# Kernel optimization log

Measured on AMD Instinct MI355X. Metric: run time of the kernel, lower is better.

## Reference

```python
import jax, jax.numpy as jnp
import numpy as np

N = 16384          # number of nodes
FEAT = 256         # in_features
POOL_RATIO = 0.5
K = max(2, int(POOL_RATIO * N))  # 8192, static


def setup_inputs() -> dict:
    key = jax.random.key(0)
    k1, k2, k3 = jax.random.split(key, 3)
    x = jax.random.normal(k1, (N, FEAT), dtype=jnp.float32)
    # dense proxy for the adjacency matrix (source calls A.todense())
    A = jax.random.uniform(k2, (N, N), dtype=jnp.float32)
    # fc: Linear(FEAT, 1, bias=None) -> weight vector of shape [FEAT]
    W = jax.random.normal(k3, (FEAT,), dtype=jnp.float32) * (1.0 / np.sqrt(FEAT))
    return {"x": x, "A": A, "W": W}


def reference(x, A, W):
    # score = fc(dropout(x)); dropout p=0 -> identity
    score = x @ W                                   # [N]
    # global L2 normalization: score / sqrt(sum(score**2))
    score = score / jnp.sqrt(jnp.sum(score * score))
    score = jnp.tanh(score)                         # activation_gPool
    values, idx = jax.lax.top_k(score, K)           # [K], [K]
    new_x = x[idx, :] * values[:, None]             # gather + scale  [K, FEAT]
    new_A = A[idx, :][:, idx]                       # [K, K] subgraph adjacency
    return new_x, new_A, idx
```

## Files before the change

kernel.cpp:

```cpp
#include <hip/hip_runtime.h>
#include <hip/hip_bf16.h>

#define N     16384
#define FEAT  256
#define KSEL  8192
#define NCHUNK 8
#define CHUNK (N / NCHUNK)

typedef float f32x4 __attribute__((ext_vector_type(4)));

__device__ __align__(16) double g_s[N];
__device__ __align__(16) int    g_cnt[N];
__device__ __align__(16) int    g_sel[KSEL];
__device__ __align__(16) float  g_vals[KSEL];
__device__              double  g_norminv;

static __device__ __forceinline__ unsigned long long mono_key(double s) {
    unsigned long long u = (unsigned long long)__double_as_longlong(s);
    if (u & 0x8000000000000000ull) u = ~u;
    else                           u |= 0x8000000000000000ull;
    return u;
}

__global__ __launch_bounds__(512) void k_score(const float* __restrict__ x,
                                               const float* __restrict__ W) {
    int lane = threadIdx.x & 63;
    int row  = blockIdx.x * 8 + (threadIdx.x >> 6);
    float4 xv = reinterpret_cast<const float4*>(x)[row * 64 + lane];
    float4 wv = reinterpret_cast<const float4*>(W)[lane];
    double acc = (double)xv.x * (double)wv.x + (double)xv.y * (double)wv.y
               + (double)xv.z * (double)wv.z + (double)xv.w * (double)wv.w;
    #pragma unroll
    for (int m = 32; m >= 1; m >>= 1) acc += __shfl_xor(acc, m, 64);
    if (lane == 0) { g_s[row] = acc; g_cnt[row] = 0; }
}

__global__ __launch_bounds__(1024) void k_norm() {
    __shared__ double red[1024];
    double acc = 0.0;
    for (int j = threadIdx.x; j < N; j += 1024) { double v = g_s[j]; acc += v * v; }
    red[threadIdx.x] = acc;
    __syncthreads();
    for (int w = 512; w >= 1; w >>= 1) {
        if ((int)threadIdx.x < w) red[threadIdx.x] += red[threadIdx.x + w];
        __syncthreads();
    }
    if (threadIdx.x == 0) g_norminv = 1.0 / sqrt(red[0]);
}

__global__ void k_rank() {
    __shared__ unsigned long long lk[CHUNK];
    int i = blockIdx.x * 256 + threadIdx.x;
    int jbase = blockIdx.y * CHUNK;
    for (int t = threadIdx.x; t < CHUNK; t += 256) lk[t] = mono_key(g_s[jbase + t]);
    __syncthreads();
    unsigned long long ki = mono_key(g_s[i]);
    int c = 0;
    #pragma unroll 4
    for (int jj = 0; jj < CHUNK; ++jj) {
        unsigned long long kj = lk[jj];
        c += (int)((kj > ki) | ((kj == ki) & ((jbase + jj) < i)));
    }
    atomicAdd(&g_cnt[i], c);
}

__global__ void k_select(float* __restrict__ out_idx) {
    int i = blockIdx.x * 256 + threadIdx.x;
    int r = g_cnt[i];
    if ((unsigned)r < (unsigned)KSEL) {
        g_sel[r]    = i;
        g_vals[r]   = (float)tanh(g_s[i] * g_norminv);
        out_idx[r]  = (float)i;
    }
}

__global__ __launch_bounds__(512) void k_gather(const float* __restrict__ x,
                                                const float* __restrict__ A,
                                                f32x4* __restrict__ outx,
                                                f32x4* __restrict__ outA) {
    __shared__ unsigned short rowb[N];
    int r = blockIdx.x;
    int srcr = g_sel[r] & (N - 1);

    if (threadIdx.x < 64) {
        float v = g_vals[r];
        f32x4 xv = reinterpret_cast<const f32x4*>(x + (size_t)srcr * FEAT)[threadIdx.x];
        outx[(size_t)r * (FEAT / 4) + threadIdx.x] = xv * v;
    }

    const f32x4* src = reinterpret_cast<const f32x4*>(A + (size_t)srcr * N);
    uint2* rb = reinterpret_cast<uint2*>(rowb);
    #pragma unroll
    for (int it = 0; it < (N / 4) / 512; ++it) {
        int t = it * 512 + threadIdx.x;
        f32x4 a = __builtin_nontemporal_load(src + t);
        uint2 p;
        p.x = (__float_as_uint(a.y) & 0xFFFF0000u) | (__float_as_uint(a.x) >> 16);
        p.y = (__float_as_uint(a.w) & 0xFFFF0000u) | (__float_as_uint(a.z) >> 16);
        rb[t] = p;
    }
    __syncthreads();

    const int4* sel4 = reinterpret_cast<const int4*>(g_sel);
    #pragma unroll
    for (int it = 0; it < (KSEL / 4) / 512; ++it) {
        int c4 = it * 512 + threadIdx.x;
        int4 cc = sel4[c4];
        f32x4 o;
        o.x = __uint_as_float((unsigned)rowb[cc.x & (N - 1)] << 16);
        o.y = __uint_as_float((unsigned)rowb[cc.y & (N - 1)] << 16);
        o.z = __uint_as_float((unsigned)rowb[cc.z & (N - 1)] << 16);
        o.w = __uint_as_float((unsigned)rowb[cc.w & (N - 1)] << 16);
        __builtin_nontemporal_store(o, outA + (size_t)r * (KSEL / 4) + c4);
    }
}

extern "C" void kernel_launch(void* const* d_in, const int* in_sizes, int n_in,
                              void* d_out, int out_size, void* d_ws, size_t ws_size,
                              hipStream_t stream) {
    const float* x = nullptr; const float* A = nullptr; const float* W = nullptr;
    for (int i = 0; i < n_in; ++i) {
        if      (in_sizes[i] == N * FEAT) x = (const float*)d_in[i];
        else if (in_sizes[i] == N * N)    A = (const float*)d_in[i];
        else if (in_sizes[i] == FEAT)     W = (const float*)d_in[i];
    }
    if (!x || !A || !W) return;

    float* out = (float*)d_out;
    float* out_x   = out;
    float* out_A   = out + (size_t)KSEL * FEAT;
    float* out_idx = out + (size_t)out_size - KSEL;

    hipLaunchKernelGGL(k_score, dim3(N / 8), dim3(512), 0, stream, x, W);
    hipLaunchKernelGGL(k_norm, dim3(1), dim3(1024), 0, stream);
    hipLaunchKernelGGL(k_rank, dim3(N / 256, NCHUNK), dim3(256), 0, stream);
    hipLaunchKernelGGL(k_select, dim3(N / 256), dim3(256), 0, stream, out_idx);
    hipLaunchKernelGGL(k_gather, dim3(KSEL), dim3(512), 0, stream,
                       x, A, (f32x4*)out_x, (f32x4*)out_A);
}
```

Measured before the change: 218.5 us.

## Fuse score, norm, rank and select into one cooperative kernel with grid syncs

Replaces four separate launches (score, norm, rank, select) with a single cooperative kernel that uses grid-wide syncs between phases. The norm becomes a two-level reduction over per-block partials. Ranking now compares doubles directly instead of monotonic integer keys, and uses 16 column chunks of 1024 each. This removes launch gaps and the single-block norm kernel, but grid syncs cost something and the cooperative grid of 1024 blocks must be fully co-resident.

Measured after the change: 404.2 us. +85.0%, slower.

```diff
diff --git a/kernel.cpp b/kernel.cpp
--- a/kernel.cpp
+++ b/kernel.cpp
@@ -1,76 +1,86 @@
 #include <hip/hip_runtime.h>
 #include <hip/hip_bf16.h>
+#include <hip/hip_cooperative_groups.h>
+
+namespace cg = cooperative_groups;
 
 #define N     16384
 #define FEAT  256
 #define KSEL  8192
-#define NCHUNK 8
-#define CHUNK (N / NCHUNK)
 
 typedef float f32x4 __attribute__((ext_vector_type(4)));
 
 __device__ __align__(16) double g_s[N];
+__device__ __align__(16) double g_part[1024];
 __device__ __align__(16) int    g_cnt[N];
 __device__ __align__(16) int    g_sel[KSEL];
 __device__ __align__(16) float  g_vals[KSEL];
 __device__              double  g_norminv;
 
-static __device__ __forceinline__ unsigned long long mono_key(double s) {
-    unsigned long long u = (unsigned long long)__double_as_longlong(s);
-    if (u & 0x8000000000000000ull) u = ~u;
-    else                           u |= 0x8000000000000000ull;
-    return u;
-}
+__global__ __launch_bounds__(256) void k_front(const float* __restrict__ x,
+                                               const float* __restrict__ W,
+                                               float* __restrict__ out_idx) {
+    const int tid  = threadIdx.x;
+    const int lane = tid & 63;
+    const int wv   = tid >> 6;
+    const int b    = blockIdx.x;
+    __shared__ double s_rows[16];
+    __shared__ double lk[1024];
 
-__global__ __launch_bounds__(512) void k_score(const float* __restrict__ x,
-                                               const float* __restrict__ W) {
-    int lane = threadIdx.x & 63;
-    int row  = blockIdx.x * 8 + (threadIdx.x >> 6);
-    float4 xv = reinterpret_cast<const float4*>(x)[row * 64 + lane];
-    float4 wv = reinterpret_cast<const float4*>(W)[lane];
-    double acc = (double)xv.x * (double)wv.x + (double)xv.y * (double)wv.y
-               + (double)xv.z * (double)wv.z + (double)xv.w * (double)wv.w;
-    #pragma unroll
-    for (int m = 32; m >= 1; m >>= 1) acc += __shfl_xor(acc, m, 64);
-    if (lane == 0) { g_s[row] = acc; g_cnt[row] = 0; }
-}
+    {
+        float4 wvec = reinterpret_cast<const float4*>(W)[lane];
+        #pragma unroll
+        for (int k = 0; k < 4; ++k) {
+            int row = b * 16 + wv * 4 + k;
+            float4 xv = reinterpret_cast<const float4*>(x)[row * 64 + lane];
+            double acc = (double)xv.x * (double)wvec.x + (double)xv.y * (double)wvec.y
+                       + (double)xv.z * (double)wvec.z + (double)xv.w * (double)wvec.w;
+            #pragma unroll
+            for (int m = 32; m >= 1; m >>= 1) acc += __shfl_xor(acc, m, 64);
+            if (lane == 0) { g_s[row] = acc; g_cnt[row] = 0; s_rows[wv * 4 + k] = acc; }
+        }
+    }
+    __syncthreads();
+    if (tid == 0) {
+        double p = 0.0;
+        #pragma unroll
+        for (int k = 0; k < 16; ++k) { double v = s_rows[k]; p += v * v; }
+        g_part[b] = p;
+    }
+    cg::this_grid().sync();
 
-__global__ __launch_bounds__(1024) void k_norm() {
-    __shared__ double red[1024];
-    double acc = 0.0;
-    for (int j = threadIdx.x; j < N; j += 1024) { double v = g_s[j]; acc += v * v; }
-    red[threadIdx.x] = acc;
-    __syncthreads();
-    for (int w = 512; w >= 1; w >>= 1) {
-        if ((int)threadIdx.x < w) red[threadIdx.x] += red[threadIdx.x + w];
+    if (b == 0 && wv == 0) {
+        double acc = 0.0;
+        #pragma unroll
+        for (int k = 0; k < 16; ++k) acc += g_part[lane + k * 64];
+        #pragma unroll
+        for (int m = 32; m >= 1; m >>= 1) acc += __shfl_xor(acc, m, 64);
+        if (lane == 0) g_norminv = 1.0 / sqrt(acc);
+    }
+    {
+        int i = (b & 63) * 256 + tid;
+        int jbase = (b >> 6) * 1024;
+        for (int t = tid; t < 1024; t += 256) lk[t] = g_s[jbase + t];
         __syncthreads();
+        double si = g_s[i];
+        int c = 0;
+        #pragma unroll 8
+        for (int jj = 0; jj < 1024; ++jj) {
+            double sj = lk[jj];
+            c += (int)((sj > si) | ((sj == si) & ((jbase + jj) < i)));
+        }
+        atomicAdd(&g_cnt[i], c);
     }
-    if (threadIdx.x == 0) g_norminv = 1.0 / sqrt(red[0]);
-}
+    cg::this_grid().sync();
 
-__global__ void k_rank() {
-    __shared__ unsigned long long lk[CHUNK];
-    int i = blockIdx.x * 256 + threadIdx.x;
-    int jbase = blockIdx.y * CHUNK;
-    for (int t = threadIdx.x; t < CHUNK; t += 256) lk[t] = mono_key(g_s[jbase + t]);
-    __syncthreads();
-    unsigned long long ki = mono_key(g_s[i]);
-    int c = 0;
-    #pragma unroll 4
-    for (int jj = 0; jj < CHUNK; ++jj) {
-        unsigned long long kj = lk[jj];
-        c += (int)((kj > ki) | ((kj == ki) & ((jbase + jj) < i)));
-    }
-    atomicAdd(&g_cnt[i], c);
-}
-
-__global__ void k_select(float* __restrict__ out_idx) {
-    int i = blockIdx.x * 256 + threadIdx.x;
-    int r = g_cnt[i];
-    if ((unsigned)r < (unsigned)KSEL) {
-        g_sel[r]    = i;
-        g_vals[r]   = (float)tanh(g_s[i] * g_norminv);
-        out_idx[r]  = (float)i;
+    if (b < 64) {
+        int i = b * 256 + tid;
+        int r = g_cnt[i];
+        if ((unsigned)r < (unsigned)KSEL) {
+            g_sel[r]   = i;
+            g_vals[r]  = tanhf((float)(g_s[i] * g_norminv));
+            out_idx[r] = (float)i;
+        }
     }
 }
 
@@ -131,10 +141,8 @@
     float* out_A   = out + (size_t)KSEL * FEAT;
     float* out_idx = out + (size_t)out_size - KSEL;
 
-    hipLaunchKernelGGL(k_score, dim3(N / 8), dim3(512), 0, stream, x, W);
-    hipLaunchKernelGGL(k_norm, dim3(1), dim3(1024), 0, stream);
-    hipLaunchKernelGGL(k_rank, dim3(N / 256, NCHUNK), dim3(256), 0, stream);
-    hipLaunchKernelGGL(k_select, dim3(N / 256), dim3(256), 0, stream, out_idx);
+    void* args[] = { (void*)&x, (void*)&W, (void*)&out_idx };
+    hipLaunchCooperativeKernel((void*)k_front, dim3(1024), dim3(256), args, 0, stream);
     hipLaunchKernelGGL(k_gather, dim3(KSEL), dim3(512), 0, stream,
                        x, A, (f32x4*)out_x, (f32x4*)out_A);
 }
```
